# Optimization experiments

Hardware: AMD Instinct MI355X
Metric: run time of the kernel (lower is better)

The kernel has to match this reference:

```python
import jax, jax.numpy as jnp
import numpy as np
from jax import lax


def setup_inputs() -> dict:
    key = jax.random.key(0)
    k1, k2 = jax.random.split(key)
    B, T, C = 8, 4096, 256
    UNITS, WINDOW = 256, 2
    x = jax.random.normal(k1, (B, T, C), dtype=jnp.float32)
    kernel = jax.random.normal(k2, (WINDOW, C, 3 * UNITS), dtype=jnp.float32) * 0.05
    bias = jnp.zeros((3 * UNITS,), dtype=jnp.float32)
    return {"x": x, "kernel": kernel, "bias": bias}


def _qrnn_forward(x, kernel, bias):
    # Causal conv1d: left-pad time axis by (window - 1).
    window = kernel.shape[0]
    xp = jnp.pad(x, ((0, 0), (window - 1, 0), (0, 0)))
    gates = lax.conv_general_dilated(
        xp, kernel, window_strides=(1,), padding='VALID',
        dimension_numbers=('NWC', 'WIO', 'NWC')) + bias
    z, f, o = jnp.split(gates, 3, axis=-1)  # each [B, T, units]
    z = jnp.tanh(z)
    f = jax.nn.sigmoid(f)

    # fo_pool: c_t = f_t * c_{t-1} + (1 - f_t) * z_t, c_0 = 0.
    # Linear recurrence -> associative scan over time with elements (a, b):
    # compose((a1,b1),(a2,b2)) = (a1*a2, a2*b1 + b2).
    def combine(e1, e2):
        a1, b1 = e1
        a2, b2 = e2
        return a1 * a2, a2 * b1 + b2

    _, c = lax.associative_scan(combine, (f, (1.0 - f) * z), axis=1)
    h = jax.nn.sigmoid(o) * c  # output gate
    return h  # return_sequences=True -> [B, T, units]


def reference(x, kernel, bias):
    return _qrnn_forward(x, kernel, bias)
```

## Files before the change

### kernel.cpp

```cpp
#include <hip/hip_runtime.h>
#include <math.h>


#define Bq 8
#define Tq 4096
#define NCq 64
#define Lq 64

typedef __attribute__((ext_vector_type(8))) _Float16 f16x8;
typedef __attribute__((ext_vector_type(4))) float f32x4;

__device__ __forceinline__ float sigmoidf_(float x) {
    return 1.f / (1.f + __expf(-x));
}
__device__ __forceinline__ float tanh_fast(float x) {
    return 1.f - 2.f / (__expf(2.f * x) + 1.f);
}
__device__ __forceinline__ unsigned short f16b(float a) {
    _Float16 h = (_Float16)a;
    return *(unsigned short*)&h;
}
__device__ __forceinline__ void gload16(const void* g, void* l) {
    __builtin_amdgcn_global_load_lds(
        (const __attribute__((address_space(1))) void*)g,
        (__attribute__((address_space(3))) void*)l, 16, 0, 0);
}

__global__ __launch_bounds__(256) void split_xk(
    const float* __restrict__ x, const float* __restrict__ kw,
    _Float16* __restrict__ xh, _Float16* __restrict__ bh)
{
    const int NX = Bq * 4097 * 64;
    int idx = blockIdx.x * 256 + threadIdx.x;
    if (idx < NX) {
        int b  = idx / (4097 * 64);
        int r  = idx % (4097 * 64);
        int tp = r / 64, c4 = (r % 64) << 2;
        size_t o = ((size_t)(b * 4097 + tp) << 8) + c4;
        _Float16 h4[4] = {(_Float16)0.f, (_Float16)0.f, (_Float16)0.f, (_Float16)0.f};
        if (tp > 0) {
            const float4 v = *(const float4*)&x[((size_t)(b * 4096 + tp - 1) << 8) + c4];
            h4[0] = (_Float16)v.x; h4[1] = (_Float16)v.y;
            h4[2] = (_Float16)v.z; h4[3] = (_Float16)v.w;
        }
        *(ushort4*)&xh[o] = *(ushort4*)h4;
    } else {
        int j = idx - NX;
        if (j < 768 * 512) {
            int n = j >> 9, k = j & 511;
            bh[((size_t)n << 9) + k] = (_Float16)kw[(size_t)k * 768 + n];
        }
    }
}

__global__ __launch_bounds__(256, 2) void conv_gemm(
    const _Float16* __restrict__ xh, const _Float16* __restrict__ bth,
    const float* __restrict__ bias,
    _Float16* __restrict__ Z, _Float16* __restrict__ G, _Float16* __restrict__ SO)
{
    __shared__ __align__(16) char smem[65536];
    const int tid = threadIdx.x;
    const int l = tid & 63, w = tid >> 6;
    const int wr = w >> 1, wc = w & 1;
    const int lg = l >> 4, l15 = l & 15;
    const int bm = blockIdx.x;
    const int by = blockIdx.y;
    const int b  = bm >> 5;
    const int t0 = (bm & 31) << 7;
    const int n0 = by << 8;

    f32x4 acc[4][8] = {};

    const int rowT   = tid >> 2;
    const int slotSw = (tid & 3) ^ ((rowT >> 1) & 3);
    size_t gaBase = ((size_t)(b * 4097 + t0 + rowT) << 8) + (slotSw << 3);
    size_t gbBase = ((size_t)(n0 + rowT) << 9) + (slotSw << 3);
    const int ldsW = w << 10;

    int offA[4], offB[8];
    #pragma unroll
    for (int i = 0; i < 4; ++i) {
        int ra = wr * 64 + i * 16 + l15;
        offA[i] = ((ra << 6) + (lg << 4)) ^ (((ra >> 1) & 3) << 4);
    }
    #pragma unroll
    for (int i = 0; i < 8; ++i) {
        int rb = wc * 128 + i * 16 + l15;
        offB[i] = ((rb << 6) + (lg << 4)) ^ (((rb >> 1) & 3) << 4);
    }

    auto stage = [&](int buf, int kk) {
        char* bA = smem + buf * 24576;
        char* bB = bA + 8192;
        size_t ga = gaBase + (size_t)kk * 32;
        size_t gb = gbBase + (size_t)kk * 32;
        #pragma unroll
        for (int g = 0; g < 2; ++g)
            gload16(xh + ga + (size_t)g * 16384, bA + g * 4096 + ldsW);
        #pragma unroll
        for (int g = 0; g < 4; ++g)
            gload16(bth + gb + (size_t)g * 32768, bB + g * 4096 + ldsW);
    };

    auto compute = [&](int buf) {
        const char* bA = smem + buf * 24576;
        const char* bB = bA + 8192;
        f16x8 fa[4], fb[8];
        #pragma unroll
        for (int i = 0; i < 4; ++i) fa[i] = *(const f16x8*)(bA + offA[i]);
        #pragma unroll
        for (int i = 0; i < 8; ++i) fb[i] = *(const f16x8*)(bB + offB[i]);
        __builtin_amdgcn_s_setprio(1);
        #pragma unroll
        for (int mi = 0; mi < 4; ++mi)
            #pragma unroll
            for (int ni = 0; ni < 8; ++ni)
                acc[mi][ni] = __builtin_amdgcn_mfma_f32_16x16x32_f16(
                    fa[mi], fb[ni], acc[mi][ni], 0, 0, 0);
        __builtin_amdgcn_s_setprio(0);
    };

    stage(0, 0);
    __syncthreads();
    int buf = 0;
    #pragma unroll
    for (int kk = 0; kk < 16; ++kk) {
        if (kk < 15) stage(buf ^ 1, kk + 1);
        compute(buf);
        __syncthreads();
        buf ^= 1;
    }

    const int gsel = by;
    float bb[8];
    #pragma unroll
    for (int ni = 0; ni < 8; ++ni)
        bb[ni] = bias[n0 + wc * 128 + ni * 16 + l15];

    unsigned short* Hd = (unsigned short*)smem;
    #pragma unroll
    for (int ni = 0; ni < 8; ++ni) {
        const int cl = wc * 128 + ni * 16 + l15;
        #pragma unroll
        for (int mi = 0; mi < 4; ++mi)
            #pragma unroll
            for (int r = 0; r < 4; ++r) {
                const int trl = wr * 64 + mi * 16 + lg * 4 + r;
                float g = acc[mi][ni][r] + bb[ni];
                float a = (gsel == 0) ? tanh_fast(g)
                        : (gsel == 1) ? sigmoidf_(-g)
                                      : sigmoidf_(g);
                int byt = (trl << 9) + ((cl << 1) ^ (((trl >> 2) & 3) << 4));
                *(unsigned short*)((char*)Hd + byt) = f16b(a);
            }
    }
    __syncthreads();
    _Float16* Gg = (gsel == 0) ? Z : (gsel == 1) ? G : SO;
    const size_t gbase = ((size_t)(b * 4096 + t0)) << 8;
    #pragma unroll
    for (int i = 0; i < 16; ++i) {
        int off = (i * 256 + tid) << 4;
        int row = off >> 9;
        int cby = off & 511;
        int src = (row << 9) + (cby ^ (((row >> 2) & 3) << 4));
        int4 v = *(const int4*)((const char*)Hd + src);
        *(int4*)&Gg[gbase + ((size_t)row << 8) + (cby >> 1)] = v;
    }
}

__global__ __launch_bounds__(256) void chunk_reduce(
    const _Float16* __restrict__ Z, const _Float16* __restrict__ G,
    float* __restrict__ CA, float* __restrict__ CB)
{
    const int u = threadIdx.x;
    const int blk = blockIdx.x;
    const int b = blk >> 6, ck = blk & 63;
    size_t base = (((size_t)b << 12) + ck * Lq) * 256 + u;
    float A = 1.f, Bv = 0.f;
    #pragma unroll 8
    for (int s = 0; s < Lq; ++s) {
        size_t idx = base + (size_t)s * 256;
        float g = (float)G[idx];
        float z = (float)Z[idx];
        Bv = fmaf(1.f - g, Bv, g * z);
        A *= (1.f - g);
    }
    size_t cidx = ((size_t)b * NCq + ck) * 256 + u;
    CA[cidx] = A;
    CB[cidx] = Bv;
}

__global__ __launch_bounds__(256) void carry_scan(
    const float* __restrict__ CA, const float* __restrict__ CB,
    float* __restrict__ CIN)
{
    const int u = threadIdx.x;
    const int b = blockIdx.x;
    float c = 0.f;
    #pragma unroll 8
    for (int k = 0; k < NCq; ++k) {
        size_t idx = ((size_t)b * NCq + k) * 256 + u;
        CIN[idx] = c;
        c = fmaf(CA[idx], c, CB[idx]);
    }
}

__global__ __launch_bounds__(256) void apply_scan(
    const _Float16* __restrict__ Z, const _Float16* __restrict__ G,
    const _Float16* __restrict__ SO, const float* __restrict__ CIN,
    float* __restrict__ out)
{
    const int u = threadIdx.x;
    const int blk = blockIdx.x;
    const int b = blk >> 6, ck = blk & 63;
    float c = CIN[((size_t)b * NCq + ck) * 256 + u];
    size_t base = (((size_t)b << 12) + ck * Lq) * 256 + u;
    #pragma unroll 8
    for (int s = 0; s < Lq; ++s) {
        size_t idx = base + (size_t)s * 256;
        float g = (float)G[idx], z = (float)Z[idx];
        c = fmaf(1.f - g, c, g * z);
        out[idx] = (float)SO[idx] * c;
    }
}

extern "C" void kernel_launch(void* const* d_in, const int* in_sizes, int n_in,
                              void* d_out, int out_size, void* d_ws, size_t ws_size,
                              hipStream_t stream) {
    const float* x    = (const float*)d_in[0];
    const float* kw   = (const float*)d_in[1];
    const float* bias = (const float*)d_in[2];
    float* out = (float*)d_out;

    char* p = (char*)d_ws;
    _Float16* xh  = (_Float16*)p; p += (size_t)Bq * 4097 * 256 * 2;
    _Float16* bth = (_Float16*)p; p += (size_t)768 * 512 * 2;
    _Float16* Z   = (_Float16*)p; p += (size_t)Bq * Tq * 256 * 2;
    _Float16* G   = (_Float16*)p; p += (size_t)Bq * Tq * 256 * 2;
    _Float16* SO  = (_Float16*)p; p += (size_t)Bq * Tq * 256 * 2;
    float* CA  = (float*)p; p += (size_t)Bq * NCq * 256 * 4;
    float* CB  = (float*)p; p += (size_t)Bq * NCq * 256 * 4;
    float* CIN = (float*)p;

    const int NX = Bq * 4097 * 64;
    split_xk<<<(NX + 768 * 512 + 255) / 256, 256, 0, stream>>>(x, kw, xh, bth);
    dim3 g1(256, 3);
    conv_gemm<<<g1, 256, 0, stream>>>(xh, bth, bias, Z, G, SO);
    chunk_reduce<<<512, 256, 0, stream>>>(Z, G, CA, CB);
    carry_scan<<<Bq, 256, 0, stream>>>(CA, CB, CIN);
    apply_scan<<<512, 256, 0, stream>>>(Z, G, SO, CIN, out);
}
```

Baseline: 100.8 us.

## Shrink GEMM tiles to 64x128 for more blocks and fold carry scan into apply

The conv GEMM tile drops from 128x256 to 64x128, so the grid grows from 768 to 3072 blocks with smaller LDS use and fewer accumulators per thread. This should improve occupancy and wave balance across the CUs. The separate carry_scan kernel is removed, and each apply_scan block instead recomputes its incoming carry by walking the earlier chunk summaries. That saves a launch and a serial 8-block kernel, but costs redundant loads of up to 63 chunk summaries per block and lower MFMA data reuse per block.

```diff
diff --git a/kernel.cpp b/kernel.cpp
--- a/kernel.cpp
+++ b/kernel.cpp
@@ -53,23 +53,25 @@
     }
 }
 
-__global__ __launch_bounds__(256, 2) void conv_gemm(
+__global__ __launch_bounds__(256) void conv_gemm(
     const _Float16* __restrict__ xh, const _Float16* __restrict__ bth,
     const float* __restrict__ bias,
     _Float16* __restrict__ Z, _Float16* __restrict__ G, _Float16* __restrict__ SO)
 {
-    __shared__ __align__(16) char smem[65536];
+    __shared__ __align__(16) char smem[24576];
     const int tid = threadIdx.x;
     const int l = tid & 63, w = tid >> 6;
     const int wr = w >> 1, wc = w & 1;
     const int lg = l >> 4, l15 = l & 15;
     const int bm = blockIdx.x;
     const int by = blockIdx.y;
-    const int b  = bm >> 5;
-    const int t0 = (bm & 31) << 7;
-    const int n0 = by << 8;
-
-    f32x4 acc[4][8] = {};
+    const int b  = bm >> 6;
+    const int t0 = (bm & 63) << 6;
+    const int n0 = by << 7;
+    const int gsel = by >> 1;
+    const int u0 = (by & 1) << 7;
+
+    f32x4 acc[2][4] = {};
 
     const int rowT   = tid >> 2;
     const int slotSw = (tid & 3) ^ ((rowT >> 1) & 3);
@@ -77,44 +79,42 @@
     size_t gbBase = ((size_t)(n0 + rowT) << 9) + (slotSw << 3);
     const int ldsW = w << 10;
 
-    int offA[4], offB[8];
+    int offA[2], offB[4];
+    #pragma unroll
+    for (int i = 0; i < 2; ++i) {
+        int ra = wr * 32 + i * 16 + l15;
+        offA[i] = ((ra << 6) + (lg << 4)) ^ (((ra >> 1) & 3) << 4);
+    }
     #pragma unroll
     for (int i = 0; i < 4; ++i) {
-        int ra = wr * 64 + i * 16 + l15;
-        offA[i] = ((ra << 6) + (lg << 4)) ^ (((ra >> 1) & 3) << 4);
-    }
-    #pragma unroll
-    for (int i = 0; i < 8; ++i) {
-        int rb = wc * 128 + i * 16 + l15;
+        int rb = wc * 64 + i * 16 + l15;
         offB[i] = ((rb << 6) + (lg << 4)) ^ (((rb >> 1) & 3) << 4);
     }
 
     auto stage = [&](int buf, int kk) {
-        char* bA = smem + buf * 24576;
-        char* bB = bA + 8192;
+        char* bA = smem + buf * 12288;
+        char* bB = bA + 4096;
         size_t ga = gaBase + (size_t)kk * 32;
         size_t gb = gbBase + (size_t)kk * 32;
+        gload16(xh + ga, bA + ldsW);
         #pragma unroll
         for (int g = 0; g < 2; ++g)
-            gload16(xh + ga + (size_t)g * 16384, bA + g * 4096 + ldsW);
-        #pragma unroll
-        for (int g = 0; g < 4; ++g)
             gload16(bth + gb + (size_t)g * 32768, bB + g * 4096 + ldsW);
     };
 
     auto compute = [&](int buf) {
-        const char* bA = smem + buf * 24576;
-        const char* bB = bA + 8192;
-        f16x8 fa[4], fb[8];
-        #pragma unroll
-        for (int i = 0; i < 4; ++i) fa[i] = *(const f16x8*)(bA + offA[i]);
-        #pragma unroll
-        for (int i = 0; i < 8; ++i) fb[i] = *(const f16x8*)(bB + offB[i]);
+        const char* bA = smem + buf * 12288;
+        const char* bB = bA + 4096;
+        f16x8 fa[2], fb[4];
+        #pragma unroll
+        for (int i = 0; i < 2; ++i) fa[i] = *(const f16x8*)(bA + offA[i]);
+        #pragma unroll
+        for (int i = 0; i < 4; ++i) fb[i] = *(const f16x8*)(bB + offB[i]);
         __builtin_amdgcn_s_setprio(1);
         #pragma unroll
-        for (int mi = 0; mi < 4; ++mi)
+        for (int mi = 0; mi < 2; ++mi)
             #pragma unroll
-            for (int ni = 0; ni < 8; ++ni)
+            for (int ni = 0; ni < 4; ++ni)
                 acc[mi][ni] = __builtin_amdgcn_mfma_f32_16x16x32_f16(
                     fa[mi], fb[ni], acc[mi][ni], 0, 0, 0);
         __builtin_amdgcn_s_setprio(0);
@@ -131,38 +131,37 @@
         buf ^= 1;
     }
 
-    const int gsel = by;
-    float bb[8];
-    #pragma unroll
-    for (int ni = 0; ni < 8; ++ni)
-        bb[ni] = bias[n0 + wc * 128 + ni * 16 + l15];
+    float bb[4];
+    #pragma unroll
+    for (int ni = 0; ni < 4; ++ni)
+        bb[ni] = bias[n0 + wc * 64 + ni * 16 + l15];
 
     unsigned short* Hd = (unsigned short*)smem;
     #pragma unroll
-    for (int ni = 0; ni < 8; ++ni) {
-        const int cl = wc * 128 + ni * 16 + l15;
-        #pragma unroll
-        for (int mi = 0; mi < 4; ++mi)
+    for (int ni = 0; ni < 4; ++ni) {
+        const int cl = wc * 64 + ni * 16 + l15;
+        #pragma unroll
+        for (int mi = 0; mi < 2; ++mi)
             #pragma unroll
             for (int r = 0; r < 4; ++r) {
-                const int trl = wr * 64 + mi * 16 + lg * 4 + r;
+                const int trl = wr * 32 + mi * 16 + lg * 4 + r;
                 float g = acc[mi][ni][r] + bb[ni];
                 float a = (gsel == 0) ? tanh_fast(g)
                         : (gsel == 1) ? sigmoidf_(-g)
                                       : sigmoidf_(g);
-                int byt = (trl << 9) + ((cl << 1) ^ (((trl >> 2) & 3) << 4));
+                int byt = (trl << 8) + ((cl << 1) ^ (((trl >> 2) & 3) << 4));
                 *(unsigned short*)((char*)Hd + byt) = f16b(a);
             }
     }
     __syncthreads();
     _Float16* Gg = (gsel == 0) ? Z : (gsel == 1) ? G : SO;
-    const size_t gbase = ((size_t)(b * 4096 + t0)) << 8;
-    #pragma unroll
-    for (int i = 0; i < 16; ++i) {
+    const size_t gbase = (((size_t)(b * 4096 + t0)) << 8) + u0;
+    #pragma unroll
+    for (int i = 0; i < 4; ++i) {
         int off = (i * 256 + tid) << 4;
-        int row = off >> 9;
-        int cby = off & 511;
-        int src = (row << 9) + (cby ^ (((row >> 2) & 3) << 4));
+        int row = off >> 8;
+        int cby = off & 255;
+        int src = (row << 8) + (cby ^ (((row >> 2) & 3) << 4));
         int4 v = *(const int4*)((const char*)Hd + src);
         *(int4*)&Gg[gbase + ((size_t)row << 8) + (cby >> 1)] = v;
     }
@@ -190,30 +189,19 @@
     CB[cidx] = Bv;
 }
 
-__global__ __launch_bounds__(256) void carry_scan(
-    const float* __restrict__ CA, const float* __restrict__ CB,
-    float* __restrict__ CIN)
-{
-    const int u = threadIdx.x;
-    const int b = blockIdx.x;
-    float c = 0.f;
-    #pragma unroll 8
-    for (int k = 0; k < NCq; ++k) {
-        size_t idx = ((size_t)b * NCq + k) * 256 + u;
-        CIN[idx] = c;
-        c = fmaf(CA[idx], c, CB[idx]);
-    }
-}
-
 __global__ __launch_bounds__(256) void apply_scan(
     const _Float16* __restrict__ Z, const _Float16* __restrict__ G,
-    const _Float16* __restrict__ SO, const float* __restrict__ CIN,
-    float* __restrict__ out)
+    const _Float16* __restrict__ SO, const float* __restrict__ CA,
+    const float* __restrict__ CB, float* __restrict__ out)
 {
     const int u = threadIdx.x;
     const int blk = blockIdx.x;
     const int b = blk >> 6, ck = blk & 63;
-    float c = CIN[((size_t)b * NCq + ck) * 256 + u];
+    float c = 0.f;
+    for (int k = 0; k < ck; ++k) {
+        size_t idx = ((size_t)b * NCq + k) * 256 + u;
+        c = fmaf(CA[idx], c, CB[idx]);
+    }
     size_t base = (((size_t)b << 12) + ck * Lq) * 256 + u;
     #pragma unroll 8
     for (int s = 0; s < Lq; ++s) {
@@ -239,14 +227,12 @@
     _Float16* G   = (_Float16*)p; p += (size_t)Bq * Tq * 256 * 2;
     _Float16* SO  = (_Float16*)p; p += (size_t)Bq * Tq * 256 * 2;
     float* CA  = (float*)p; p += (size_t)Bq * NCq * 256 * 4;
-    float* CB  = (float*)p; p += (size_t)Bq * NCq * 256 * 4;
-    float* CIN = (float*)p;
+    float* CB  = (float*)p;
 
     const int NX = Bq * 4097 * 64;
     split_xk<<<(NX + 768 * 512 + 255) / 256, 256, 0, stream>>>(x, kw, xh, bth);
-    dim3 g1(256, 3);
+    dim3 g1(512, 6);
     conv_gemm<<<g1, 256, 0, stream>>>(xh, bth, bias, Z, G, SO);
     chunk_reduce<<<512, 256, 0, stream>>>(Z, G, CA, CB);
-    carry_scan<<<Bq, 256, 0, stream>>>(CA, CB, CIN);
-    apply_scan<<<512, 256, 0, stream>>>(Z, G, SO, CIN, out);
-}
+    apply_scan<<<512, 256, 0, stream>>>(Z, G, SO, CA, CB, out);
+}
```

Result: faster. 92.92 us (-7.8%).
